# Kernel tuning notes

Hardware: AMD Instinct MI355X
Metric: run time of the kernel (lower is better)

Reference implementation:

```python
import jax, jax.numpy as jnp
import numpy as np

K_NUM = 3


def setup_inputs() -> dict:
    key = jax.random.key(0)
    k1, k2, k3, k4 = jax.random.split(key, 4)
    n, c_in, t, v = 16, 64, 2048, 25
    c_out = 64
    x = jax.random.normal(k1, (n, c_in, t, v), dtype=jnp.float32)
    A_skl = jax.random.uniform(k2, (K_NUM, v, v), dtype=jnp.float32)
    # nn.Linear(in_channels, out_channels * k_num): weight [k*c_out, c_in], bias [k*c_out]
    W = jax.random.normal(k3, (K_NUM * c_out, c_in), dtype=jnp.float32) * (1.0 / np.sqrt(c_in))
    b = jax.random.normal(k4, (K_NUM * c_out,), dtype=jnp.float32) * 0.01
    return {"x": x, "A_skl": A_skl, "W": W, "b": b}


def reference(x, A_skl, W, b):
    n, c_in, t, v = x.shape
    kc = W.shape[0]
    c_out = kc // K_NUM
    # permute -> Linear -> permute back, fused into one einsum over channels:
    # h[n, k*c_out, t, v] = sum_c W[o, c] * x[n, c, t, v] + b[o]
    h = jnp.einsum('nctv,oc->notv', x, W) + b[None, :, None, None]
    # view(n, k, c_out, t, v): channel dim splits as (k major, c_out minor)
    h = h.reshape(n, K_NUM, c_out, t, v)
    # graph aggregation over k adjacency subsets
    out = jnp.einsum('nkctv,kvw->nctw', h, A_skl)
    return out
```

## Files before the change

kernel.cpp:

```cpp
#include <hip/hip_runtime.h>


typedef short short8 __attribute__((ext_vector_type(8)));
typedef float floatx4 __attribute__((ext_vector_type(4)));

#define K_NUM 3
#define C_IN  64
#define C_OUT 64
#define T_DIM 2048
#define V_DIM 25
#define N_DIM 16

#define TT    2
#define NSUB  16
#define TWIN  32

#define WBUF_ELEMS (12*2*64*8)
#define ABUF_OFF   (WBUF_ELEMS*2)
#define ABUF_ELEMS (3*2*64*8)
#define B2_OFF     (ABUF_OFF + ABUF_ELEMS*2)
#define B2_ELEMS   (4*2*64*4)

__device__ __forceinline__ unsigned short bf16_rne(float f) {
    unsigned int u = __builtin_bit_cast(unsigned int, f);
    unsigned int r = (u + 0x7FFFu + ((u >> 16) & 1u)) >> 16;
    return (unsigned short)r;
}

__global__ void sgcn_prep(const float* __restrict__ W, const float* __restrict__ A,
                          const float* __restrict__ b,
                          unsigned short* __restrict__ wbuf,
                          unsigned short* __restrict__ abuf,
                          float* __restrict__ b2buf) {
    int idx = blockIdx.x * 256 + threadIdx.x;
    if (idx < WBUF_ELEMS) {
        int j = idx & 7, lane = (idx >> 3) & 63, ks = (idx >> 9) & 1, nt = idx >> 10;
        int o  = nt * 16 + (lane & 15);
        int ci = ks * 32 + ((lane >> 4) & 3) * 8 + j;
        wbuf[idx] = bf16_rne(W[o * C_IN + ci]);
    }
    if (idx < ABUF_ELEMS) {
        int j = idx & 7, lane = (idx >> 3) & 63, nt = (idx >> 9) & 1, k = idx >> 10;
        int w = nt * 16 + (lane & 15);
        int v = ((lane >> 4) & 3) * 8 + j;
        abuf[idx] = (v < V_DIM && w < V_DIM) ? bf16_rne(A[(k * V_DIM + v) * V_DIM + w])
                                             : (unsigned short)0;
    }
    if (idx < B2_ELEMS) {
        int r = idx & 3, lane = (idx >> 2) & 63, nt = (idx >> 8) & 1, mt2 = idx >> 9;
        int c = mt2 * 16 + ((lane >> 4) & 3) * 4 + r;
        int w = nt * 16 + (lane & 15);
        float val = 0.f;
        if (w < V_DIM) {
            for (int k = 0; k < K_NUM; ++k) {
                float cs = 0.f;
                for (int v = 0; v < V_DIM; ++v) cs += A[(k * V_DIM + v) * V_DIM + w];
                val += b[k * C_OUT + c] * cs;
            }
        }
        b2buf[idx] = val;
    }
}

__global__ __launch_bounds__(512)
void sgcn_main(const float* __restrict__ x,
               const unsigned short* __restrict__ wbuf,
               const unsigned short* __restrict__ abuf,
               const float* __restrict__ b2buf,
               float* __restrict__ out) {
    __shared__ __align__(16) unsigned short Xt[64 * 64];
    __shared__ __align__(16) unsigned short H2[K_NUM * TT * 64 * 32];

    const int tid  = threadIdx.x;
    const int lane = tid & 63;
    const int wid  = tid >> 6;
    const int nb   = blockIdx.x >> 6;
    const int t_base = (blockIdx.x & 63) * TWIN;

    const int wm2 = wid & 1;
    const int wq  = wid >> 1;
    const int mt2 = wid & 3, th = wid >> 2;

    short8 wfr[3][2];
    #pragma unroll
    for (int ni = 0; ni < 3; ++ni)
        #pragma unroll
        for (int ks = 0; ks < 2; ++ks)
            wfr[ni][ks] = ((const short8*)wbuf)[(((wq * 3 + ni) * 2 + ks) * 64) + lane];
    short8 afr2[3][2];
    #pragma unroll
    for (int k = 0; k < 3; ++k)
        #pragma unroll
        for (int nt = 0; nt < 2; ++nt)
            afr2[k][nt] = ((const short8*)abuf)[((k * 2 + nt) * 64) + lane];
    floatx4 b2f[2];
    b2f[0] = reinterpret_cast<const floatx4*>(b2buf)[(mt2 * 2 + 0) * 64 + lane];
    b2f[1] = reinterpret_cast<const floatx4*>(b2buf)[(mt2 * 2 + 1) * 64 + lane];

    for (int i = tid; i < 14 * 32; i += 512) {
        int pc = i >> 5, ciw = i & 31;
        int col = (pc < 7) ? (25 + pc) : (50 + pc);
        ((unsigned int*)Xt)[col * 32 + ciw] = 0u;
    }

    float xa[4], xb[4];
    const float* xptr = x + ((size_t)nb * C_IN * T_DIM + t_base) * V_DIM;

    auto LOADX = [&](int ts) {
        const float* s = xptr + ts * TT * V_DIM;
        #pragma unroll
        for (int p = 0; p < 4; ++p) {
            int u = tid + p * 512;
            if (u < 1600) {
                int ci2 = u / 50, cg = u % 50;
                size_t off = (size_t)(2 * ci2) * (T_DIM * V_DIM) + cg;
                xa[p] = s[off];
                xb[p] = s[off + T_DIM * V_DIM];
            }
        }
    };
    auto WRITEX = [&]() {
        #pragma unroll
        for (int p = 0; p < 4; ++p) {
            int u = tid + p * 512;
            if (u < 1600) {
                int ci2 = u / 50, cg = u % 50;
                int t = cg / 25, v = cg - t * 25;
                int col = t * 32 + v;
                unsigned int pk = (unsigned int)bf16_rne(xa[p]) |
                                  ((unsigned int)bf16_rne(xb[p]) << 16);
                int sw = ci2 ^ (((col >> 1) & 7) << 2);
                ((unsigned int*)Xt)[col * 32 + sw] = pk;
            }
        }
    };

    LOADX(0);

    #pragma unroll 1
    for (int ts = 0; ts < NSUB; ++ts) {
        WRITEX();
        __syncthreads();

        short8 xfr[2][2];
        #pragma unroll
        for (int mi = 0; mi < 2; ++mi) {
            int acol = (wm2 * 2 + mi) * 16 + (lane & 15);
            #pragma unroll
            for (int ks = 0; ks < 2; ++ks) {
                int blk = (ks * 4 + ((lane >> 4) & 3)) ^ ((acol >> 1) & 7);
                xfr[mi][ks] = *(const short8*)&((unsigned int*)Xt)[acol * 32 + blk * 4];
            }
        }

        if (ts + 1 < NSUB) LOADX(ts + 1);

        floatx4 acc1[2][3];
        #pragma unroll
        for (int mi = 0; mi < 2; ++mi)
            #pragma unroll
            for (int ni = 0; ni < 3; ++ni)
                acc1[mi][ni] = floatx4{0.f, 0.f, 0.f, 0.f};

        #pragma unroll
        for (int mi = 0; mi < 2; ++mi)
            #pragma unroll
            for (int ni = 0; ni < 3; ++ni)
                #pragma unroll
                for (int ks = 0; ks < 2; ++ks)
                    acc1[mi][ni] = __builtin_amdgcn_mfma_f32_16x16x32_bf16(
                        xfr[mi][ks], wfr[ni][ks], acc1[mi][ni], 0, 0, 0);

        #pragma unroll
        for (int mi = 0; mi < 2; ++mi) {
            int vb = mi * 16 + ((lane >> 4) & 3) * 4;
            #pragma unroll
            for (int ni = 0; ni < 3; ++ni) {
                int o = wq * 48 + ni * 16 + (lane & 15);
                int k = o >> 6, c = o & 63;
                int swv = vb ^ (((c >> 2) & 3) << 3);
                unsigned long long lo =
                    (unsigned long long)((unsigned int)bf16_rne(acc1[mi][ni][0]) |
                                         ((unsigned int)bf16_rne(acc1[mi][ni][1]) << 16));
                unsigned long long hi =
                    (unsigned long long)((unsigned int)bf16_rne(acc1[mi][ni][2]) |
                                         ((unsigned int)bf16_rne(acc1[mi][ni][3]) << 16));
                int idx16 = ((k * TT + wm2) * 64 + c) * 32 + swv;
                ((unsigned long long*)H2)[idx16 >> 2] = lo | (hi << 32);
            }
        }
        __syncthreads();

        floatx4 acc2[2];
        acc2[0] = b2f[0];
        acc2[1] = b2f[1];
        const int c_a = mt2 * 16 + (lane & 15);
        #pragma unroll
        for (int k = 0; k < K_NUM; ++k) {
            int row = (k * TT + th) * 64 + c_a;
            int blk = ((lane >> 4) & 3) ^ ((c_a >> 2) & 3);
            short8 ha = *(const short8*)&((unsigned int*)H2)[row * 16 + blk * 4];
            #pragma unroll
            for (int nt = 0; nt < 2; ++nt)
                acc2[nt] = __builtin_amdgcn_mfma_f32_16x16x32_bf16(
                    ha, afr2[k][nt], acc2[nt], 0, 0, 0);
        }

        const int tg = t_base + ts * TT + th;
        const int c0 = mt2 * 16 + ((lane >> 4) & 3) * 4;
        const int wl = lane & 15;
        #pragma unroll
        for (int r = 0; r < 4; ++r)
            out[((size_t)(nb * C_OUT + c0 + r) * T_DIM + tg) * V_DIM + wl] = acc2[0][r];
        if (wl < 9) {
            #pragma unroll
            for (int r = 0; r < 4; ++r)
                out[((size_t)(nb * C_OUT + c0 + r) * T_DIM + tg) * V_DIM + 16 + wl] = acc2[1][r];
        }
    }
}

extern "C" void kernel_launch(void* const* d_in, const int* in_sizes, int n_in,
                              void* d_out, int out_size, void* d_ws, size_t ws_size,
                              hipStream_t stream) {
    const float* x = (const float*)d_in[0];
    const float* A = (const float*)d_in[1];
    const float* W = (const float*)d_in[2];
    const float* b = (const float*)d_in[3];
    float* out = (float*)d_out;

    unsigned short* wbuf = (unsigned short*)d_ws;
    unsigned short* abuf = (unsigned short*)((char*)d_ws + ABUF_OFF);
    float* b2buf = (float*)((char*)d_ws + B2_OFF);

    sgcn_prep<<<(WBUF_ELEMS + 255) / 256, 256, 0, stream>>>(W, A, b, wbuf, abuf, b2buf);

    dim3 grid(N_DIM * (T_DIM / TWIN));
    sgcn_main<<<grid, 512, 0, stream>>>(x, wbuf, abuf, b2buf, out);
}
```

Before: 127.0 us.

## Software-pipeline stages with double-buffered LDS and one barrier per step

Double-buffers the X tile and the intermediate H tile in shared memory so that the second GEMM for step ts-1 overlaps the first GEMM for step ts. This drops one __syncthreads per iteration. The x load is also reorganised so 400 threads each load 8 channels and write one 16-byte packed LDS store, prefetched two steps ahead. The cost is twice the LDS footprint, more live registers, and lower occupancy, and fewer threads now issue global loads.

```diff
diff --git a/kernel.cpp b/kernel.cpp
--- a/kernel.cpp
+++ b/kernel.cpp
@@ -3,6 +3,7 @@
 
 typedef short short8 __attribute__((ext_vector_type(8)));
 typedef float floatx4 __attribute__((ext_vector_type(4)));
+typedef unsigned int uintx4 __attribute__((ext_vector_type(4)));
 
 #define K_NUM 3
 #define C_IN  64
@@ -14,6 +15,7 @@
 #define TT    2
 #define NSUB  16
 #define TWIN  32
+#define XROW  51200
 
 #define WBUF_ELEMS (12*2*64*8)
 #define ABUF_OFF   (WBUF_ELEMS*2)
@@ -68,8 +70,8 @@
                const unsigned short* __restrict__ abuf,
                const float* __restrict__ b2buf,
                float* __restrict__ out) {
-    __shared__ __align__(16) unsigned short Xt[64 * 64];
-    __shared__ __align__(16) unsigned short H2[K_NUM * TT * 64 * 32];
+    __shared__ __align__(16) unsigned int   Xt[2][64 * 32];
+    __shared__ __align__(16) unsigned short H2[2][K_NUM * TT * 64 * 32];
 
     const int tid  = threadIdx.x;
     const int lane = tid & 63;
@@ -97,125 +99,132 @@
     b2f[0] = reinterpret_cast<const floatx4*>(b2buf)[(mt2 * 2 + 0) * 64 + lane];
     b2f[1] = reinterpret_cast<const floatx4*>(b2buf)[(mt2 * 2 + 1) * 64 + lane];
 
-    for (int i = tid; i < 14 * 32; i += 512) {
-        int pc = i >> 5, ciw = i & 31;
+    for (int i = tid; i < 2 * 14 * 32; i += 512) {
+        int bsel = i >= 14 * 32;
+        int j = i - bsel * 14 * 32;
+        int pc = j >> 5, ciw = j & 31;
         int col = (pc < 7) ? (25 + pc) : (50 + pc);
-        ((unsigned int*)Xt)[col * 32 + ciw] = 0u;
-    }
-
-    float xa[4], xb[4];
+        Xt[bsel][col * 32 + ciw] = 0u;
+    }
+
+    float xq[8];
     const float* xptr = x + ((size_t)nb * C_IN * T_DIM + t_base) * V_DIM;
+    const int ciq = tid / 50, cg = tid % 50;
+    const int icol = (cg / 25) * 32 + (cg % 25);
+    const int isw  = (ciq ^ ((icol >> 1) & 7)) * 4;
 
     auto LOADX = [&](int ts) {
-        const float* s = xptr + ts * TT * V_DIM;
-        #pragma unroll
-        for (int p = 0; p < 4; ++p) {
-            int u = tid + p * 512;
-            if (u < 1600) {
-                int ci2 = u / 50, cg = u % 50;
-                size_t off = (size_t)(2 * ci2) * (T_DIM * V_DIM) + cg;
-                xa[p] = s[off];
-                xb[p] = s[off + T_DIM * V_DIM];
-            }
+        if (tid < 400) {
+            const float* s = xptr + ts * (TT * V_DIM) + (size_t)(ciq * 8) * XROW + cg;
+            #pragma unroll
+            for (int r = 0; r < 8; ++r) xq[r] = s[(size_t)r * XROW];
         }
     };
-    auto WRITEX = [&]() {
-        #pragma unroll
-        for (int p = 0; p < 4; ++p) {
-            int u = tid + p * 512;
-            if (u < 1600) {
-                int ci2 = u / 50, cg = u % 50;
-                int t = cg / 25, v = cg - t * 25;
-                int col = t * 32 + v;
-                unsigned int pk = (unsigned int)bf16_rne(xa[p]) |
-                                  ((unsigned int)bf16_rne(xb[p]) << 16);
-                int sw = ci2 ^ (((col >> 1) & 7) << 2);
-                ((unsigned int*)Xt)[col * 32 + sw] = pk;
-            }
+    auto WRITEX = [&](int bsel) {
+        if (tid < 400) {
+            uintx4 pk;
+            #pragma unroll
+            for (int j = 0; j < 4; ++j)
+                pk[j] = (unsigned int)bf16_rne(xq[2 * j]) |
+                        ((unsigned int)bf16_rne(xq[2 * j + 1]) << 16);
+            *reinterpret_cast<uintx4*>(&Xt[bsel][icol * 32 + isw]) = pk;
         }
     };
 
     LOADX(0);
+    WRITEX(0);
+    LOADX(1);
 
     #pragma unroll 1
-    for (int ts = 0; ts < NSUB; ++ts) {
-        WRITEX();
+    for (int ts = 0; ts <= NSUB; ++ts) {
         __syncthreads();
-
+        const int cur = ts & 1, prv = 1 - cur;
+
+        floatx4 acc1[2][3];
         short8 xfr[2][2];
-        #pragma unroll
-        for (int mi = 0; mi < 2; ++mi) {
-            int acol = (wm2 * 2 + mi) * 16 + (lane & 15);
-            #pragma unroll
-            for (int ks = 0; ks < 2; ++ks) {
-                int blk = (ks * 4 + ((lane >> 4) & 3)) ^ ((acol >> 1) & 7);
-                xfr[mi][ks] = *(const short8*)&((unsigned int*)Xt)[acol * 32 + blk * 4];
-            }
-        }
-
-        if (ts + 1 < NSUB) LOADX(ts + 1);
-
-        floatx4 acc1[2][3];
-        #pragma unroll
-        for (int mi = 0; mi < 2; ++mi)
-            #pragma unroll
-            for (int ni = 0; ni < 3; ++ni)
-                acc1[mi][ni] = floatx4{0.f, 0.f, 0.f, 0.f};
-
-        #pragma unroll
-        for (int mi = 0; mi < 2; ++mi)
-            #pragma unroll
-            for (int ni = 0; ni < 3; ++ni)
-                #pragma unroll
-                for (int ks = 0; ks < 2; ++ks)
-                    acc1[mi][ni] = __builtin_amdgcn_mfma_f32_16x16x32_bf16(
-                        xfr[mi][ks], wfr[ni][ks], acc1[mi][ni], 0, 0, 0);
-
-        #pragma unroll
-        for (int mi = 0; mi < 2; ++mi) {
-            int vb = mi * 16 + ((lane >> 4) & 3) * 4;
-            #pragma unroll
-            for (int ni = 0; ni < 3; ++ni) {
-                int o = wq * 48 + ni * 16 + (lane & 15);
-                int k = o >> 6, c = o & 63;
-                int swv = vb ^ (((c >> 2) & 3) << 3);
-                unsigned long long lo =
-                    (unsigned long long)((unsigned int)bf16_rne(acc1[mi][ni][0]) |
-                                         ((unsigned int)bf16_rne(acc1[mi][ni][1]) << 16));
-                unsigned long long hi =
-                    (unsigned long long)((unsigned int)bf16_rne(acc1[mi][ni][2]) |
-                                         ((unsigned int)bf16_rne(acc1[mi][ni][3]) << 16));
-                int idx16 = ((k * TT + wm2) * 64 + c) * 32 + swv;
-                ((unsigned long long*)H2)[idx16 >> 2] = lo | (hi << 32);
-            }
-        }
-        __syncthreads();
-
-        floatx4 acc2[2];
-        acc2[0] = b2f[0];
-        acc2[1] = b2f[1];
-        const int c_a = mt2 * 16 + (lane & 15);
-        #pragma unroll
-        for (int k = 0; k < K_NUM; ++k) {
-            int row = (k * TT + th) * 64 + c_a;
-            int blk = ((lane >> 4) & 3) ^ ((c_a >> 2) & 3);
-            short8 ha = *(const short8*)&((unsigned int*)H2)[row * 16 + blk * 4];
-            #pragma unroll
-            for (int nt = 0; nt < 2; ++nt)
-                acc2[nt] = __builtin_amdgcn_mfma_f32_16x16x32_bf16(
-                    ha, afr2[k][nt], acc2[nt], 0, 0, 0);
-        }
-
-        const int tg = t_base + ts * TT + th;
-        const int c0 = mt2 * 16 + ((lane >> 4) & 3) * 4;
-        const int wl = lane & 15;
-        #pragma unroll
-        for (int r = 0; r < 4; ++r)
-            out[((size_t)(nb * C_OUT + c0 + r) * T_DIM + tg) * V_DIM + wl] = acc2[0][r];
-        if (wl < 9) {
+        if (ts < NSUB) {
+            #pragma unroll
+            for (int mi = 0; mi < 2; ++mi) {
+                int acol = (wm2 * 2 + mi) * 16 + (lane & 15);
+                #pragma unroll
+                for (int ks = 0; ks < 2; ++ks) {
+                    int blk = (ks * 4 + ((lane >> 4) & 3)) ^ ((acol >> 1) & 7);
+                    xfr[mi][ks] = *(const short8*)&Xt[cur][acol * 32 + blk * 4];
+                }
+            }
+        }
+
+        short8 ha[3];
+        if (ts >= 1) {
+            const int c_a = mt2 * 16 + (lane & 15);
+            #pragma unroll
+            for (int k = 0; k < K_NUM; ++k) {
+                int row = (k * TT + th) * 64 + c_a;
+                int blk = ((lane >> 4) & 3) ^ ((c_a >> 2) & 3);
+                ha[k] = *(const short8*)&((const unsigned int*)H2[prv])[row * 16 + blk * 4];
+            }
+        }
+
+        if (ts + 1 < NSUB) WRITEX(cur ^ 1);
+        if (ts + 2 < NSUB) LOADX(ts + 2);
+
+        if (ts < NSUB) {
+            #pragma unroll
+            for (int mi = 0; mi < 2; ++mi)
+                #pragma unroll
+                for (int ni = 0; ni < 3; ++ni)
+                    acc1[mi][ni] = floatx4{0.f, 0.f, 0.f, 0.f};
+            #pragma unroll
+            for (int mi = 0; mi < 2; ++mi)
+                #pragma unroll
+                for (int ni = 0; ni < 3; ++ni)
+                    #pragma unroll
+                    for (int ks = 0; ks < 2; ++ks)
+                        acc1[mi][ni] = __builtin_amdgcn_mfma_f32_16x16x32_bf16(
+                            xfr[mi][ks], wfr[ni][ks], acc1[mi][ni], 0, 0, 0);
+
+            #pragma unroll
+            for (int mi = 0; mi < 2; ++mi) {
+                int vb = mi * 16 + ((lane >> 4) & 3) * 4;
+                #pragma unroll
+                for (int ni = 0; ni < 3; ++ni) {
+                    int o = wq * 48 + ni * 16 + (lane & 15);
+                    int k = o >> 6, c = o & 63;
+                    int swv = vb ^ (((c >> 2) & 3) << 3);
+                    unsigned long long lo =
+                        (unsigned long long)((unsigned int)bf16_rne(acc1[mi][ni][0]) |
+                                             ((unsigned int)bf16_rne(acc1[mi][ni][1]) << 16));
+                    unsigned long long hi =
+                        (unsigned long long)((unsigned int)bf16_rne(acc1[mi][ni][2]) |
+                                             ((unsigned int)bf16_rne(acc1[mi][ni][3]) << 16));
+                    int idx16 = ((k * TT + wm2) * 64 + c) * 32 + swv;
+                    ((unsigned long long*)H2[cur])[idx16 >> 2] = lo | (hi << 32);
+                }
+            }
+        }
+
+        if (ts >= 1) {
+            floatx4 acc2[2];
+            acc2[0] = b2f[0];
+            acc2[1] = b2f[1];
+            #pragma unroll
+            for (int k = 0; k < K_NUM; ++k)
+                #pragma unroll
+                for (int nt = 0; nt < 2; ++nt)
+                    acc2[nt] = __builtin_amdgcn_mfma_f32_16x16x32_bf16(
+                        ha[k], afr2[k][nt], acc2[nt], 0, 0, 0);
+
+            const int tg = t_base + (ts - 1) * TT + th;
+            const int c0 = mt2 * 16 + ((lane >> 4) & 3) * 4;
+            const int wl = lane & 15;
             #pragma unroll
             for (int r = 0; r < 4; ++r)
-                out[((size_t)(nb * C_OUT + c0 + r) * T_DIM + tg) * V_DIM + 16 + wl] = acc2[1][r];
+                out[((size_t)(nb * C_OUT + c0 + r) * T_DIM + tg) * V_DIM + wl] = acc2[0][r];
+            if (wl < 9) {
+                #pragma unroll
+                for (int r = 0; r < 4; ++r)
+                    out[((size_t)(nb * C_OUT + c0 + r) * T_DIM + tg) * V_DIM + 16 + wl] = acc2[1][r];
+            }
         }
     }
 }
```

After: 122.9 us. 1.03x faster.
